# Performance work log

Measured on AMD Instinct MI355X. Metric: run time of the kernel, lower is better.

## Reference

```python
import jax, jax.numpy as jnp
import numpy as np

N, T, E, D, U = 32, 2048, 512, 1024, 256


def setup_inputs() -> dict:
    key = jax.random.key(0)
    ks = jax.random.split(key, 6)
    queries = jax.random.normal(ks[0], (N, 1, D), dtype=jnp.float32)
    prev = jax.random.uniform(ks[1], (N, T), dtype=jnp.float32)
    prev = prev / jnp.sum(prev, axis=1, keepdims=True)  # distribution-like initial alignment
    memory = jax.random.normal(ks[2], (N, T, E), dtype=jnp.float32)
    W_q = jax.random.normal(ks[3], (D, U), dtype=jnp.float32) * (1.0 / np.sqrt(D))
    W_k = jax.random.normal(ks[4], (E, U), dtype=jnp.float32) * (1.0 / np.sqrt(E))
    v = jax.random.uniform(ks[5], (U,), dtype=jnp.float32)
    return {"queries": queries, "previous_alignments": prev, "memory": memory,
            "W_q": W_q, "W_k": W_k, "v": v}


def safe_cumprod_exclusive(x):
    # exclusive cumprod via log-space cumsum, clamped like the torch original
    logsum = jnp.cumsum(jnp.log(jnp.clip(x, 1e-20, 1.0)), axis=1)  # [N,T]
    excl = jnp.concatenate([jnp.zeros_like(logsum[:, :1]), logsum], axis=1)[:, :-1]
    return jnp.exp(excl)


def reference(queries, previous_alignments, memory, W_q, W_k, v):
    # Bahdanau additive score (normalize=False path)
    proj_key = jnp.einsum('bte,eu->btu', memory, W_k)          # set_memory
    proj_q = jnp.einsum('bqd,du->bqu', queries, W_q)           # [N,1,U]
    weights = jnp.einsum('btu,u->bt', jnp.tanh(proj_q + proj_key), v)  # [N,T]
    p_choose = jax.nn.sigmoid(weights)
    # monotonic attention recursion in cumsum/cumprod form
    cumprod_1mp = safe_cumprod_exclusive(1.0 - p_choose)
    alignments = p_choose * cumprod_1mp * jnp.cumsum(
        previous_alignments / jnp.clip(cumprod_1mp, 1e-10, 1.0), axis=1)
    contexts = jnp.einsum('bt,bte->be', alignments, memory)    # bmm + squeeze
    return (contexts, alignments)
```

## Files before the change

### kernel.cpp

```cpp
#include <hip/hip_runtime.h>
#include <math.h>

#define N_ 32
#define T_ 2048
#define E_ 512
#define D_ 1024
#define U_ 256

typedef __attribute__((ext_vector_type(8))) short bf16x8;
typedef __attribute__((ext_vector_type(16))) float f32x16;

__device__ __forceinline__ short f2bf_rne(float x) {
  unsigned int u = __float_as_uint(x);
  unsigned int r = u + 0x7FFFu + ((u >> 16) & 1u);
  return (short)(r >> 16);
}
__device__ __forceinline__ short f2bf_trunc(float x) {
  return (short)(__float_as_uint(x) >> 16);
}
__device__ __forceinline__ float bf2f(short h) {
  return __uint_as_float(((unsigned int)(unsigned short)h) << 16);
}
__device__ __forceinline__ float fast_tanh(float x) {
  float t = exp2f(x * 2.8853900817779268f);
  return 1.0f - 2.0f * __builtin_amdgcn_rcpf(t + 1.0f);
}
__device__ __forceinline__ float fast_sigmoid(float w) {
  return __builtin_amdgcn_rcpf(1.0f + exp2f(-1.4426950408889634f * w));
}

__global__ __launch_bounds__(256) void prep_kernel(
    const float* __restrict__ Wk, const float* __restrict__ queries,
    const float* __restrict__ Wq, bf16x8* __restrict__ whiP,
    bf16x8* __restrict__ wloP, float* __restrict__ pq_part) {
  const int wg = blockIdx.x, tid = threadIdx.x;
  if (wg < 64) {
    const int fid = wg * 256 + tid;
    const int lane = fid & 63;
    const int ub = (fid >> 6) & 7;
    const int kc = (fid >> 9) & 3;
    const int c = fid >> 11;
    const int u = ub * 32 + (lane & 31);
    const int e0 = c * 64 + kc * 16 + (lane >> 5) * 8;
    bf16x8 H, L;
#pragma unroll
    for (int j = 0; j < 8; ++j) {
      float x = Wk[(size_t)(e0 + j) * U_ + u];
      short h = f2bf_trunc(x);
      H[j] = h;
      L[j] = f2bf_rne(x - bf2f(h));
    }
    whiP[fid] = H;
    wloP[fid] = L;
  } else {
    const int ch = (wg - 64) & 3;
    const int bb = (wg - 64) >> 2;
    const int d0 = ch * 256;
    const float* q = queries + bb * D_ + d0;
    const float* wq = Wq + (size_t)d0 * U_ + tid;
    float acc = 0.f;
#pragma unroll 8
    for (int d = 0; d < 256; ++d)
      acc = fmaf(q[d], wq[(size_t)d * U_], acc);
    pq_part[(bb * 4 + ch) * U_ + tid] = acc;
  }
}

__global__ __launch_bounds__(256, 2) void score_kernel(
    const float* __restrict__ memory, const bf16x8* __restrict__ whiP,
    const bf16x8* __restrict__ wloP, const float* __restrict__ pq_part,
    const float* __restrict__ v, float* __restrict__ p_choose) {
  __shared__ float smem_w[4][128];

  const int b = blockIdx.y;
  const int t0 = blockIdx.x * 128;
  const int tid = threadIdx.x;
  const int lane = tid & 63;
  const int ty = tid >> 6;
  const int l31 = lane & 31;
  const int half = lane >> 5;

  f32x16 acc[4][2];
#pragma unroll
  for (int mt = 0; mt < 4; ++mt)
#pragma unroll
    for (int nt = 0; nt < 2; ++nt)
#pragma unroll
      for (int r = 0; r < 16; ++r) acc[mt][nt][r] = 0.f;

  const float* aptr = memory + ((size_t)(b * T_ + t0 + l31)) * E_ + half * 8;
  const bf16x8* bhp = whiP + (size_t)(ty * 2) * 64 + lane;
  const bf16x8* blp = wloP + (size_t)(ty * 2) * 64 + lane;

#pragma unroll 2
  for (int step = 0; step < 32; ++step) {
    float4 a0[4], a1[4];
#pragma unroll
    for (int mt = 0; mt < 4; ++mt) {
      const float* p = aptr + (size_t)mt * (32 * E_) + step * 16;
      a0[mt] = *(const float4*)(p);
      a1[mt] = *(const float4*)(p + 4);
    }
    bf16x8 bh[2], bl[2];
#pragma unroll
    for (int nt = 0; nt < 2; ++nt) {
      bh[nt] = bhp[(size_t)(step * 8 + nt) * 64];
      bl[nt] = blp[(size_t)(step * 8 + nt) * 64];
    }
    bf16x8 ah[4], al[4];
#pragma unroll
    for (int mt = 0; mt < 4; ++mt) {
      float xs[8] = {a0[mt].x, a0[mt].y, a0[mt].z, a0[mt].w,
                     a1[mt].x, a1[mt].y, a1[mt].z, a1[mt].w};
#pragma unroll
      for (int i = 0; i < 8; ++i) {
        short h = f2bf_trunc(xs[i]);
        ah[mt][i] = h;
        al[mt][i] = f2bf_rne(xs[i] - bf2f(h));
      }
    }
#pragma unroll
    for (int mt = 0; mt < 4; ++mt)
#pragma unroll
      for (int nt = 0; nt < 2; ++nt) {
        acc[mt][nt] = __builtin_amdgcn_mfma_f32_32x32x16_bf16(ah[mt], bh[nt], acc[mt][nt], 0, 0, 0);
        acc[mt][nt] = __builtin_amdgcn_mfma_f32_32x32x16_bf16(ah[mt], bl[nt], acc[mt][nt], 0, 0, 0);
        acc[mt][nt] = __builtin_amdgcn_mfma_f32_32x32x16_bf16(al[mt], bh[nt], acc[mt][nt], 0, 0, 0);
      }
  }

  const int u0 = ty * 64 + l31;
  const int u1 = u0 + 32;
  float pq0 = 0.f, pq1 = 0.f;
#pragma unroll
  for (int c = 0; c < 4; ++c) {
    pq0 += pq_part[(b * 4 + c) * U_ + u0];
    pq1 += pq_part[(b * 4 + c) * U_ + u1];
  }
  const float v0 = v[u0], v1 = v[u1];
#pragma unroll
  for (int mt = 0; mt < 4; ++mt)
#pragma unroll
    for (int r = 0; r < 16; ++r) {
      float s = fast_tanh(acc[mt][0][r] + pq0) * v0 + fast_tanh(acc[mt][1][r] + pq1) * v1;
#pragma unroll
      for (int off = 1; off < 32; off <<= 1) s += __shfl_xor(s, off, 64);
      if (l31 == 0) {
        const int row = mt * 32 + (r & 3) + 8 * (r >> 2) + 4 * half;
        smem_w[ty][row] = s;
      }
    }
  __syncthreads();
  if (tid < 128) {
    const float w = smem_w[0][tid] + smem_w[1][tid] + smem_w[2][tid] + smem_w[3][tid];
    p_choose[b * T_ + t0 + tid] = fast_sigmoid(w);
  }
}

__device__ __forceinline__ float block_incl_scan(float val, float* sbuf, int tid) {
  float x = val;
  sbuf[tid] = x;
  __syncthreads();
#pragma unroll
  for (int off = 1; off < 256; off <<= 1) {
    float t = (tid >= off) ? sbuf[tid - off] : 0.f;
    __syncthreads();
    x += t;
    sbuf[tid] = x;
    __syncthreads();
  }
  return x;
}

__global__ __launch_bounds__(256) void scan_kernel(
    const float* __restrict__ p_choose, const float* __restrict__ prev,
    float* __restrict__ align_out, float* __restrict__ ctx_out) {
  __shared__ float sbuf[256];
  const int b = blockIdx.x, tid = threadIdx.x;
  ctx_out[b * E_ + tid] = 0.f;
  ctx_out[b * E_ + 256 + tid] = 0.f;
  const int base = b * T_ + tid * 8;
  float4 p0 = *(const float4*)(p_choose + base);
  float4 p1 = *(const float4*)(p_choose + base + 4);
  float p[8] = {p0.x, p0.y, p0.z, p0.w, p1.x, p1.y, p1.z, p1.w};
  float s[8];
  float run = 0.f;
#pragma unroll
  for (int k = 0; k < 8; ++k) {
    float x = 1.0f - p[k];
    x = fminf(fmaxf(x, 1e-20f), 1.0f);
    run += logf(x);
    s[k] = run;
  }
  float incl = block_incl_scan(run, sbuf, tid);
  float excl = incl - run;
  float cp[8];
#pragma unroll
  for (int k = 0; k < 8; ++k)
    cp[k] = expf(excl + (k ? s[k - 1] : 0.f));
  float4 r0 = *(const float4*)(prev + base);
  float4 r1 = *(const float4*)(prev + base + 4);
  float pr[8] = {r0.x, r0.y, r0.z, r0.w, r1.x, r1.y, r1.z, r1.w};
  float s2[8];
  float run2 = 0.f;
#pragma unroll
  for (int k = 0; k < 8; ++k) {
    float d = fminf(fmaxf(cp[k], 1e-10f), 1.0f);
    run2 += pr[k] / d;
    s2[k] = run2;
  }
  float incl2 = block_incl_scan(run2, sbuf, tid);
  float excl2 = incl2 - run2;
#pragma unroll
  for (int k = 0; k < 8; ++k)
    p[k] = p[k] * cp[k] * (excl2 + s2[k]);
  *(float4*)(align_out + base) = make_float4(p[0], p[1], p[2], p[3]);
  *(float4*)(align_out + base + 4) = make_float4(p[4], p[5], p[6], p[7]);
}

__global__ __launch_bounds__(256) void ctx_kernel(
    const float* __restrict__ memory, const float* __restrict__ align,
    float* __restrict__ ctx_out) {
  const int wg = blockIdx.x, tid = threadIdx.x;
  const int b = wg >> 4;
  const int t0 = (wg & 15) * 128 + (tid >> 7) * 64;
  const int col = (tid & 127) * 4;
  const float* mrow = memory + ((size_t)(b * T_ + t0)) * E_ + col;
  const float* arow = align + b * T_ + t0;
  float4 a = make_float4(0.f, 0.f, 0.f, 0.f);
  for (int t = 0; t < 64; t += 4) {
    float4 m0 = *(const float4*)(mrow + (size_t)(t + 0) * E_);
    float4 m1 = *(const float4*)(mrow + (size_t)(t + 1) * E_);
    float4 m2 = *(const float4*)(mrow + (size_t)(t + 2) * E_);
    float4 m3 = *(const float4*)(mrow + (size_t)(t + 3) * E_);
    float a0 = arow[t], a1 = arow[t + 1], a2 = arow[t + 2], a3 = arow[t + 3];
    a.x = fmaf(a0, m0.x, a.x); a.y = fmaf(a0, m0.y, a.y);
    a.z = fmaf(a0, m0.z, a.z); a.w = fmaf(a0, m0.w, a.w);
    a.x = fmaf(a1, m1.x, a.x); a.y = fmaf(a1, m1.y, a.y);
    a.z = fmaf(a1, m1.z, a.z); a.w = fmaf(a1, m1.w, a.w);
    a.x = fmaf(a2, m2.x, a.x); a.y = fmaf(a2, m2.y, a.y);
    a.z = fmaf(a2, m2.z, a.z); a.w = fmaf(a2, m2.w, a.w);
    a.x = fmaf(a3, m3.x, a.x); a.y = fmaf(a3, m3.y, a.y);
    a.z = fmaf(a3, m3.z, a.z); a.w = fmaf(a3, m3.w, a.w);
  }
  float* dst = ctx_out + b * E_ + col;
  atomicAdd(dst + 0, a.x);
  atomicAdd(dst + 1, a.y);
  atomicAdd(dst + 2, a.z);
  atomicAdd(dst + 3, a.w);
}

extern "C" void kernel_launch(void* const* d_in, const int* in_sizes, int n_in,
                              void* d_out, int out_size, void* d_ws, size_t ws_size,
                              hipStream_t stream) {
  (void)in_sizes; (void)n_in; (void)out_size; (void)ws_size;
  const float* queries = (const float*)d_in[0];
  const float* prev    = (const float*)d_in[1];
  const float* memory  = (const float*)d_in[2];
  const float* Wq      = (const float*)d_in[3];
  const float* Wk      = (const float*)d_in[4];
  const float* v       = (const float*)d_in[5];

  float* out = (float*)d_out;
  float* ctx_out = out;
  float* align_out = out + N_ * E_;

  float* ws = (float*)d_ws;
  bf16x8* whiP    = (bf16x8*)ws;
  bf16x8* wloP    = (bf16x8*)(ws + 65536);
  float* p_choose = ws + 131072;
  float* pq_part  = ws + 196608;

  prep_kernel<<<dim3(64 + 128), 256, 0, stream>>>(Wk, queries, Wq, whiP, wloP, pq_part);
  score_kernel<<<dim3(T_ / 128, N_), 256, 0, stream>>>(memory, whiP, wloP, pq_part, v, p_choose);
  scan_kernel<<<dim3(N_), 256, 0, stream>>>(p_choose, prev, align_out, ctx_out);
  ctx_kernel<<<dim3(512), 256, 0, stream>>>(memory, align_out, ctx_out);
}
```

Baseline: 316.1 us.

## Stage memory tiles through LDS with async global_load_lds double buffering

The score kernel now loads each 128x32 fp32 tile of memory straight into shared memory with global_load_lds, double-buffered so the next tile's load overlaps the current tile's MFMA work. Previously every wave loaded the same A rows directly from global memory, four times per block. The LDS layout uses an XOR swizzle to avoid bank conflicts on the per-lane float4 reads. This adds 32 KB of LDS per block and a barrier per iteration, which may limit occupancy under launch_bounds(256,2).

```diff
diff --git a/kernel.cpp b/kernel.cpp
--- a/kernel.cpp
+++ b/kernel.cpp
@@ -27,6 +27,12 @@
 }
 __device__ __forceinline__ float fast_sigmoid(float w) {
   return __builtin_amdgcn_rcpf(1.0f + exp2f(-1.4426950408889634f * w));
+}
+
+__device__ __forceinline__ void gload_lds16(const float* src, void* dst) {
+  __builtin_amdgcn_global_load_lds(
+      (const __attribute__((address_space(1))) void*)src,
+      (__attribute__((address_space(3))) void*)dst, 16, 0, 0);
 }
 
 __global__ __launch_bounds__(256) void prep_kernel(
@@ -70,6 +76,7 @@
     const float* __restrict__ memory, const bf16x8* __restrict__ whiP,
     const bf16x8* __restrict__ wloP, const float* __restrict__ pq_part,
     const float* __restrict__ v, float* __restrict__ p_choose) {
+  __shared__ float sAf[2][128 * 32];
   __shared__ float smem_w[4][128];
 
   const int b = blockIdx.y;
@@ -88,45 +95,66 @@
 #pragma unroll
       for (int r = 0; r < 16; ++r) acc[mt][nt][r] = 0.f;
 
-  const float* aptr = memory + ((size_t)(b * T_ + t0 + l31)) * E_ + half * 8;
-  const bf16x8* bhp = whiP + (size_t)(ty * 2) * 64 + lane;
-  const bf16x8* blp = wloP + (size_t)(ty * 2) * 64 + lane;
-
-#pragma unroll 2
-  for (int step = 0; step < 32; ++step) {
-    float4 a0[4], a1[4];
-#pragma unroll
-    for (int mt = 0; mt < 4; ++mt) {
-      const float* p = aptr + (size_t)mt * (32 * E_) + step * 16;
-      a0[mt] = *(const float4*)(p);
-      a1[mt] = *(const float4*)(p + 4);
+  const float* gsrc[4];
+  int ldsoff[4];
+#pragma unroll
+  for (int i = 0; i < 4; ++i) {
+    const int C = (ty * 4 + i) * 64 + lane;
+    const int r = C >> 3;
+    const int sl = (C & 7) ^ (r & 7);
+    gsrc[i] = memory + ((size_t)(b * T_ + t0 + r)) * E_ + sl * 4;
+    ldsoff[i] = (ty * 4 + i) * 1024;
+  }
+
+  auto do_stage = [&](int buf, int itn) {
+    const int co = itn * 32;
+#pragma unroll
+    for (int i = 0; i < 4; ++i)
+      gload_lds16(gsrc[i] + co, (char*)&sAf[buf][0] + ldsoff[i]);
+  };
+
+  do_stage(0, 0);
+  __syncthreads();
+
+  for (int it = 0; it < 16; ++it) {
+    if (it < 15) do_stage((it + 1) & 1, it + 1);
+
+    const char* base = (const char*)&sAf[it & 1][0];
+#pragma unroll
+    for (int kc = 0; kc < 2; ++kc) {
+      bf16x8 bh[2], bl[2];
+#pragma unroll
+      for (int nt = 0; nt < 2; ++nt) {
+        const int fidx = ((it * 2 + kc) * 8 + (ty * 2 + nt)) * 64 + lane;
+        bh[nt] = whiP[fidx];
+        bl[nt] = wloP[fidx];
+      }
+      const int ls0 = half * 2 + kc * 4;
+      bf16x8 ah[4], al[4];
+#pragma unroll
+      for (int mt = 0; mt < 4; ++mt) {
+        const int m = mt * 32 + l31;
+        const char* rowp = base + (size_t)m * 128;
+        float4 f0 = *(const float4*)(rowp + ((ls0 ^ (m & 7)) * 16));
+        float4 f1 = *(const float4*)(rowp + (((ls0 + 1) ^ (m & 7)) * 16));
+        float xs[8] = {f0.x, f0.y, f0.z, f0.w, f1.x, f1.y, f1.z, f1.w};
+#pragma unroll
+        for (int i = 0; i < 8; ++i) {
+          short h = f2bf_trunc(xs[i]);
+          ah[mt][i] = h;
+          al[mt][i] = f2bf_rne(xs[i] - bf2f(h));
+        }
+      }
+#pragma unroll
+      for (int mt = 0; mt < 4; ++mt)
+#pragma unroll
+        for (int nt = 0; nt < 2; ++nt) {
+          acc[mt][nt] = __builtin_amdgcn_mfma_f32_32x32x16_bf16(ah[mt], bh[nt], acc[mt][nt], 0, 0, 0);
+          acc[mt][nt] = __builtin_amdgcn_mfma_f32_32x32x16_bf16(ah[mt], bl[nt], acc[mt][nt], 0, 0, 0);
+          acc[mt][nt] = __builtin_amdgcn_mfma_f32_32x32x16_bf16(al[mt], bh[nt], acc[mt][nt], 0, 0, 0);
+        }
     }
-    bf16x8 bh[2], bl[2];
-#pragma unroll
-    for (int nt = 0; nt < 2; ++nt) {
-      bh[nt] = bhp[(size_t)(step * 8 + nt) * 64];
-      bl[nt] = blp[(size_t)(step * 8 + nt) * 64];
-    }
-    bf16x8 ah[4], al[4];
-#pragma unroll
-    for (int mt = 0; mt < 4; ++mt) {
-      float xs[8] = {a0[mt].x, a0[mt].y, a0[mt].z, a0[mt].w,
-                     a1[mt].x, a1[mt].y, a1[mt].z, a1[mt].w};
-#pragma unroll
-      for (int i = 0; i < 8; ++i) {
-        short h = f2bf_trunc(xs[i]);
-        ah[mt][i] = h;
-        al[mt][i] = f2bf_rne(xs[i] - bf2f(h));
-      }
-    }
-#pragma unroll
-    for (int mt = 0; mt < 4; ++mt)
-#pragma unroll
-      for (int nt = 0; nt < 2; ++nt) {
-        acc[mt][nt] = __builtin_amdgcn_mfma_f32_32x32x16_bf16(ah[mt], bh[nt], acc[mt][nt], 0, 0, 0);
-        acc[mt][nt] = __builtin_amdgcn_mfma_f32_32x32x16_bf16(ah[mt], bl[nt], acc[mt][nt], 0, 0, 0);
-        acc[mt][nt] = __builtin_amdgcn_mfma_f32_32x32x16_bf16(al[mt], bh[nt], acc[mt][nt], 0, 0, 0);
-      }
+    __syncthreads();
   }
 
   const int u0 = ty * 64 + l31;
```

New measurement: 272.5 us. 13.8% less time.
